# Kernel tuning notes

Measured on AMD Instinct MI355X. Metric: run time of the kernel, lower is better.

The kernel has to match this reference:

```python
import jax, jax.numpy as jnp
import numpy as np
import math

B, T, C, NH = 4, 2048, 1024, 16
HS = C // NH  # 64

def rope_cache(dim, max_pos):
    half = dim // 2
    inv_freq = 1.0 / (10000.0 ** (jnp.arange(half, dtype=jnp.float32) * 2.0 / dim))
    ang = jnp.arange(max_pos, dtype=jnp.float32)[:, None] * inv_freq[None, :]
    return jnp.cos(ang), jnp.sin(ang)  # each [T, half]

def apply_rope(x, cos, sin):
    # x: [B, nH, T, hs]; rotate consecutive pairs (complex multiply)
    x0 = x[..., 0::2]
    x1 = x[..., 1::2]
    c = cos[None, None, :, :]
    s = sin[None, None, :, :]
    r0 = x0 * c - x1 * s
    r1 = x0 * s + x1 * c
    return jnp.stack([r0, r1], axis=-1).reshape(x.shape)

def setup_inputs() -> dict:
    key = jax.random.key(0)
    ks = jax.random.split(key, 5)
    sc = 1.0 / math.sqrt(C)
    return {
        "x": jax.random.normal(ks[0], (B, T, C), jnp.float32),
        "Wq": jax.random.normal(ks[1], (C, C), jnp.float32) * sc,
        "bq": jnp.zeros((C,), jnp.float32),
        "Wk": jax.random.normal(ks[2], (C, C), jnp.float32) * sc,
        "bk": jnp.zeros((C,), jnp.float32),
        "Wv": jax.random.normal(ks[3], (C, C), jnp.float32) * sc,
        "bv": jnp.zeros((C,), jnp.float32),
        "Wp": jax.random.normal(ks[4], (C, C), jnp.float32) * sc,
        "bp": jnp.zeros((C,), jnp.float32),
    }

def reference(x, Wq, bq, Wk, bk, Wv, bv, Wp, bp):
    Bx, Tx, Cx = x.shape
    def split_heads(y):
        return y.reshape(Bx, Tx, NH, HS).transpose(0, 2, 1, 3)  # [B,nH,T,hs]
    q = split_heads(x @ Wq + bq)
    k = split_heads(x @ Wk + bk)
    v = split_heads(x @ Wv + bv)
    cos, sin = rope_cache(HS, Tx)
    q = apply_rope(q, cos, sin)
    k = apply_rope(k, cos, sin)
    att = jnp.einsum("bhqd,bhkd->bhqk", q, k) * (1.0 / math.sqrt(HS))
    causal = jnp.tril(jnp.ones((Tx, Tx), bool))
    att = jnp.where(causal[None, None, :, :], att, jnp.float32(-1e10))
    att = jax.nn.softmax(att, axis=-1)
    y = jnp.einsum("bhqk,bhkd->bhqd", att, v)
    y = y.transpose(0, 2, 1, 3).reshape(Bx, Tx, Cx)
    return y @ Wp + bp
```

## Files before the change

### kernel.cpp

```cpp
#include <hip/hip_runtime.h>
#include <math.h>

#define B_  4
#define T_  2048
#define C_  1024
#define NH_ 16
#define HS_ 64
#define M_  (B_ * T_)
#define BH_ (B_ * NH_)

typedef __bf16 bf16_t;
typedef __bf16 bf16x8 __attribute__((ext_vector_type(8)));
typedef float  f32x4  __attribute__((ext_vector_type(4)));

__device__ __forceinline__ f32x4 mfma16(bf16x8 a, bf16x8 b, f32x4 c) {
    return __builtin_amdgcn_mfma_f32_16x16x32_bf16(a, b, c, 0, 0, 0);
}

#define GLOAD16(gp, lp) __builtin_amdgcn_global_load_lds( \
    (const __attribute__((address_space(1))) void*)(gp),  \
    (__attribute__((address_space(3))) void*)(lp), 16, 0, 0)


__global__ void cvt_x(const float* __restrict__ x, bf16_t* __restrict__ xb) {
    int i = blockIdx.x * blockDim.x + threadIdx.x;
    const float4* src = reinterpret_cast<const float4*>(x);
    float4 u = src[2 * i], v = src[2 * i + 1];
    bf16x8 o;
    o[0] = (bf16_t)u.x; o[1] = (bf16_t)u.y; o[2] = (bf16_t)u.z; o[3] = (bf16_t)u.w;
    o[4] = (bf16_t)v.x; o[5] = (bf16_t)v.y; o[6] = (bf16_t)v.z; o[7] = (bf16_t)v.w;
    *reinterpret_cast<bf16x8*>(xb + (size_t)i * 8) = o;
}

__global__ void wtrans(const float* __restrict__ W, bf16_t* __restrict__ Wt) {
    __shared__ float tile[32][33];
    int bx = blockIdx.x, by = blockIdx.y;
    int tx = threadIdx.x, ty = threadIdx.y;
    #pragma unroll
    for (int j = 0; j < 4; ++j)
        tile[ty + j * 8][tx] = W[(size_t)(by * 32 + ty + j * 8) * 1024 + bx * 32 + tx];
    __syncthreads();
    #pragma unroll
    for (int j = 0; j < 4; ++j)
        Wt[(size_t)(bx * 32 + ty + j * 8) * 1024 + by * 32 + tx] = (bf16_t)tile[tx][ty + j * 8];
}

__global__ void rope_tab(float* __restrict__ cs, float* __restrict__ sn) {
    int idx = blockIdx.x * blockDim.x + threadIdx.x;
    int t = idx >> 5, j = idx & 31;
    float inv = 1.0f / powf(10000.0f, ((float)(2 * j)) / 64.0f);
    float ang = (float)t * inv;
    cs[idx] = cosf(ang);
    sn[idx] = sinf(ang);
}

__global__ __launch_bounds__(256) void gemm_qkv(
    const bf16_t* __restrict__ A, const bf16_t* __restrict__ Bt,
    const float* __restrict__ bq, const float* __restrict__ bk, const float* __restrict__ bv,
    bf16_t* __restrict__ outq, bf16_t* __restrict__ outk, bf16_t* __restrict__ outvt) {
    __shared__ __align__(16) bf16_t Ab[2][128 * 32];
    __shared__ __align__(16) bf16_t Bb[2][128 * 32];
    int tid = threadIdx.x;
    int lane = tid & 63, w = tid >> 6;
    int rr = lane & 15, g = lane >> 4;
    int mbase = blockIdx.y * 128;
    int nbase = blockIdx.x * 128;
    int wm = (w >> 1) * 64, wn = (w & 1) * 64;
    f32x4 acc[4][4] = {};
    int r0 = tid >> 2, c0 = tid & 3;
    const bf16_t* Asrc = A + (size_t)(mbase + r0) * 1024 + c0 * 8;
    const bf16_t* Bsrc = Bt + (size_t)(nbase + r0) * 1024 + c0 * 8;

    GLOAD16(Asrc,             &Ab[0][tid * 8]);
    GLOAD16(Asrc + 64 * 1024, &Ab[0][(tid + 256) * 8]);
    GLOAD16(Bsrc,             &Bb[0][tid * 8]);
    GLOAD16(Bsrc + 64 * 1024, &Bb[0][(tid + 256) * 8]);
    __syncthreads();
    int cur = 0;
    for (int t = 0; t < 32; ++t) {
        if (t < 31) {
            int kk = (t + 1) * 32;
            GLOAD16(Asrc + kk,             &Ab[cur ^ 1][tid * 8]);
            GLOAD16(Asrc + 64 * 1024 + kk, &Ab[cur ^ 1][(tid + 256) * 8]);
            GLOAD16(Bsrc + kk,             &Bb[cur ^ 1][tid * 8]);
            GLOAD16(Bsrc + 64 * 1024 + kk, &Bb[cur ^ 1][(tid + 256) * 8]);
        }
        bf16x8 a[4], b[4];
        #pragma unroll
        for (int i = 0; i < 4; ++i) {
            a[i] = *(const bf16x8*)&Ab[cur][(wm + i * 16 + rr) * 32 + g * 8];
            b[i] = *(const bf16x8*)&Bb[cur][(wn + i * 16 + rr) * 32 + g * 8];
        }
        #pragma unroll
        for (int mi = 0; mi < 4; ++mi)
            #pragma unroll
            for (int ni = 0; ni < 4; ++ni)
                acc[mi][ni] = mfma16(a[mi], b[ni], acc[mi][ni]);
        __syncthreads();
        cur ^= 1;
    }
    #pragma unroll
    for (int ni = 0; ni < 4; ++ni) {
        int n = nbase + wn + ni * 16 + rr;
        int sel = n >> 10, nn = n & 1023, h = nn >> 6, d = nn & 63;
        float bias = (sel == 0) ? bq[nn] : (sel == 1) ? bk[nn] : bv[nn];
        #pragma unroll
        for (int mi = 0; mi < 4; ++mi) {
            #pragma unroll
            for (int j = 0; j < 4; ++j) {
                int mrow = mbase + wm + mi * 16 + g * 4 + j;
                int bI = mrow >> 11, t = mrow & 2047;
                float val = acc[mi][ni][j] + bias;
                size_t bh = (size_t)(bI * 16 + h);
                if (sel == 0)      outq[(bh * 2048 + t) * 64 + d] = (bf16_t)val;
                else if (sel == 1) outk[(bh * 2048 + t) * 64 + d] = (bf16_t)val;
                else               outvt[(bh * 64 + d) * 2048 + t] = (bf16_t)val;
            }
        }
    }
}

__global__ void rope_qk(bf16_t* __restrict__ q, bf16_t* __restrict__ k,
                        const float* __restrict__ cs, const float* __restrict__ sn) {
    int idx = blockIdx.x * blockDim.x + threadIdx.x;
    int seg = idx & 7;
    int t = (idx >> 3) & 2047;
    int bh = idx >> 14;
    float4 cc = *reinterpret_cast<const float4*>(cs + (t << 5) + seg * 4);
    float4 ss = *reinterpret_cast<const float4*>(sn + (t << 5) + seg * 4);
    size_t base = (((size_t)bh << 11) + t) * 64 + seg * 8;
    {
        bf16x8 v = *reinterpret_cast<bf16x8*>(q + base);
        bf16x8 o;
        o[0] = (bf16_t)((float)v[0] * cc.x - (float)v[1] * ss.x);
        o[1] = (bf16_t)((float)v[0] * ss.x + (float)v[1] * cc.x);
        o[2] = (bf16_t)((float)v[2] * cc.y - (float)v[3] * ss.y);
        o[3] = (bf16_t)((float)v[2] * ss.y + (float)v[3] * cc.y);
        o[4] = (bf16_t)((float)v[4] * cc.z - (float)v[5] * ss.z);
        o[5] = (bf16_t)((float)v[4] * ss.z + (float)v[5] * cc.z);
        o[6] = (bf16_t)((float)v[6] * cc.w - (float)v[7] * ss.w);
        o[7] = (bf16_t)((float)v[6] * ss.w + (float)v[7] * cc.w);
        *reinterpret_cast<bf16x8*>(q + base) = o;
    }
    {
        bf16x8 v = *reinterpret_cast<bf16x8*>(k + base);
        bf16x8 o;
        o[0] = (bf16_t)((float)v[0] * cc.x - (float)v[1] * ss.x);
        o[1] = (bf16_t)((float)v[0] * ss.x + (float)v[1] * cc.x);
        o[2] = (bf16_t)((float)v[2] * cc.y - (float)v[3] * ss.y);
        o[3] = (bf16_t)((float)v[2] * ss.y + (float)v[3] * cc.y);
        o[4] = (bf16_t)((float)v[4] * cc.z - (float)v[5] * ss.z);
        o[5] = (bf16_t)((float)v[4] * ss.z + (float)v[5] * cc.z);
        o[6] = (bf16_t)((float)v[6] * cc.w - (float)v[7] * ss.w);
        o[7] = (bf16_t)((float)v[6] * ss.w + (float)v[7] * cc.w);
        *reinterpret_cast<bf16x8*>(k + base) = o;
    }
}

__global__ __launch_bounds__(256) void attn(
    const bf16_t* __restrict__ q, const bf16_t* __restrict__ k,
    const bf16_t* __restrict__ vt, bf16_t* __restrict__ y) {
    __shared__ __align__(16) bf16_t Kb[2][64 * 64];
    __shared__ __align__(16) bf16_t Vb[2][64 * 64];
    int tid = threadIdx.x;
    int lane = tid & 63, w = tid >> 6;
    int rr = lane & 15, g = lane >> 4;
    int bid = blockIdx.x;
    int xcd = bid & 7, idx = bid >> 3;
    int bh = xcd * 8 + (idx >> 4);
    int xp = idx & 15;
    const bf16_t* qh = q + (size_t)bh * T_ * HS_;
    const bf16_t* kh = k + (size_t)bh * T_ * HS_;
    const bf16_t* vh = vt + (size_t)bh * HS_ * T_;
    int bI = bh >> 4, h = bh & 15;
    int s0 = ((rr >> 2) << 3) + (rr & 3);
    const float SC = 0.125f * 1.44269504088896f;

    int i2a = tid, i2b = tid + 256;
    int rwa = i2a >> 3, rwb = i2b >> 3;
    int swKa = (rwa & 3) | (((rwa >> 3) & 1) << 2);
    int swKb = (rwb & 3) | (((rwb >> 3) & 1) << 2);
    int cKa = (i2a & 7) ^ swKa, cKb = (i2b & 7) ^ swKb;
    int cVa = (i2a & 7) ^ (rwa & 7), cVb = (i2b & 7) ^ (rwb & 7);

    #pragma unroll 1
    for (int pass = 0; pass < 2; ++pass) {
        int qt = pass ? (31 - xp) : xp;
        int qbase = qt * 64;
        int qrow = qbase + w * 16 + rr;
        bf16x8 qf0 = *reinterpret_cast<const bf16x8*>(qh + (size_t)qrow * 64 + g * 8);
        bf16x8 qf1 = *reinterpret_cast<const bf16x8*>(qh + (size_t)qrow * 64 + 32 + g * 8);
        float mrun = -1e30f, lsum = 0.f;
        f32x4 oacc[4] = {};
        int nt = qt + 1;
        GLOAD16(kh + (size_t)rwa * 64 + cKa * 8, &Kb[0][i2a * 8]);
        GLOAD16(kh + (size_t)rwb * 64 + cKb * 8, &Kb[0][i2b * 8]);
        GLOAD16(vh + (size_t)rwa * 2048 + cVa * 8, &Vb[0][i2a * 8]);
        GLOAD16(vh + (size_t)rwb * 2048 + cVb * 8, &Vb[0][i2b * 8]);
        __syncthreads();
        int cur = 0;
        #pragma unroll 1
        for (int t = 0; t < nt; ++t) {
            if (t + 1 < nt) {
                int kv1 = (t + 1) * 64;
                GLOAD16(kh + (size_t)(kv1 + rwa) * 64 + cKa * 8, &Kb[cur ^ 1][i2a * 8]);
                GLOAD16(kh + (size_t)(kv1 + rwb) * 64 + cKb * 8, &Kb[cur ^ 1][i2b * 8]);
                GLOAD16(vh + (size_t)rwa * 2048 + kv1 + cVa * 8, &Vb[cur ^ 1][i2a * 8]);
                GLOAD16(vh + (size_t)rwb * 2048 + kv1 + cVb * 8, &Vb[cur ^ 1][i2b * 8]);
            }
            int kv0 = t * 64;
            f32x4 st[4] = {};
            #pragma unroll
            for (int s = 0; s < 2; ++s) {
                #pragma unroll
                for (int p = 0; p < 2; ++p) {
                    int row = s * 32 + s0 + p * 4;
                    int sw = (row & 3) | (((row >> 3) & 1) << 2);
                    bf16x8 k0 = *(const bf16x8*)&Kb[cur][row * 64 + ((g ^ sw) * 8)];
                    bf16x8 k1 = *(const bf16x8*)&Kb[cur][row * 64 + (((4 + g) ^ sw) * 8)];
                    st[2 * s + p] = mfma16(k0, qf0, st[2 * s + p]);
                    st[2 * s + p] = mfma16(k1, qf1, st[2 * s + p]);
                }
            }
            float sv[16];
            #pragma unroll
            for (int s = 0; s < 2; ++s)
                #pragma unroll
                for (int p = 0; p < 2; ++p)
                    #pragma unroll
                    for (int j = 0; j < 4; ++j)
                        sv[s * 8 + p * 4 + j] = st[2 * s + p][j] * SC;
            if (t == nt - 1) {
                #pragma unroll
                for (int i = 0; i < 16; ++i) {
                    int kvi = kv0 + (i >> 3) * 32 + g * 8 + (i & 7);
                    if (kvi > qrow) sv[i] = -1e30f;
                }
            }
            float pmax = sv[0];
            #pragma unroll
            for (int i = 1; i < 16; ++i) pmax = fmaxf(pmax, sv[i]);
            pmax = fmaxf(pmax, __shfl_xor(pmax, 16));
            pmax = fmaxf(pmax, __shfl_xor(pmax, 32));
            float mnew = fmaxf(mrun, pmax);
            float fac = __builtin_amdgcn_exp2f(mrun - mnew);
            float psum = 0.f;
            bf16x8 pf0, pf1;
            #pragma unroll
            for (int i = 0; i < 8; ++i) {
                float pe = __builtin_amdgcn_exp2f(sv[i] - mnew);
                psum += pe;
                pf0[i] = (bf16_t)pe;
            }
            #pragma unroll
            for (int i = 0; i < 8; ++i) {
                float pe = __builtin_amdgcn_exp2f(sv[8 + i] - mnew);
                psum += pe;
                pf1[i] = (bf16_t)pe;
            }
            psum += __shfl_xor(psum, 16);
            psum += __shfl_xor(psum, 32);
            lsum = lsum * fac + psum;
            mrun = mnew;
            #pragma unroll
            for (int ch = 0; ch < 4; ++ch) {
                #pragma unroll
                for (int j = 0; j < 4; ++j) oacc[ch][j] *= fac;
            }
            #pragma unroll
            for (int ch = 0; ch < 4; ++ch) {
                int row = ch * 16 + rr;
                bf16x8 v0 = *(const bf16x8*)&Vb[cur][row * 64 + ((g ^ (row & 7)) * 8)];
                bf16x8 v1 = *(const bf16x8*)&Vb[cur][row * 64 + (((4 + g) ^ (row & 7)) * 8)];
                oacc[ch] = mfma16(v0, pf0, oacc[ch]);
                oacc[ch] = mfma16(v1, pf1, oacc[ch]);
            }
            __syncthreads();
            cur ^= 1;
        }
        float inv = 1.0f / lsum;
        bf16_t* yrow = y + ((size_t)bI * 2048 + qrow) * 1024 + h * 64;
        #pragma unroll
        for (int ch = 0; ch < 4; ++ch) {
            union { bf16_t b[4]; short4 s4; } u;
            #pragma unroll
            for (int j = 0; j < 4; ++j) u.b[j] = (bf16_t)(oacc[ch][j] * inv);
            *reinterpret_cast<short4*>(yrow + ch * 16 + g * 4) = u.s4;
        }
    }
}

__global__ __launch_bounds__(256) void gemm_proj(
    const bf16_t* __restrict__ A, const bf16_t* __restrict__ Bt,
    const float* __restrict__ bp, float* __restrict__ out) {
    __shared__ __align__(16) bf16_t Ab[2][128 * 32];
    __shared__ __align__(16) bf16_t Bb[2][128 * 32];
    int tid = threadIdx.x;
    int lane = tid & 63, w = tid >> 6;
    int rr = lane & 15, g = lane >> 4;
    int mbase = blockIdx.y * 128;
    int nbase = blockIdx.x * 128;
    int wm = (w >> 1) * 64, wn = (w & 1) * 64;
    f32x4 acc[4][4] = {};
    int r0 = tid >> 2, c0 = tid & 3;
    const bf16_t* Asrc = A + (size_t)(mbase + r0) * 1024 + c0 * 8;
    const bf16_t* Bsrc = Bt + (size_t)(nbase + r0) * 1024 + c0 * 8;

    GLOAD16(Asrc,             &Ab[0][tid * 8]);
    GLOAD16(Asrc + 64 * 1024, &Ab[0][(tid + 256) * 8]);
    GLOAD16(Bsrc,             &Bb[0][tid * 8]);
    GLOAD16(Bsrc + 64 * 1024, &Bb[0][(tid + 256) * 8]);
    __syncthreads();
    int cur = 0;
    for (int t = 0; t < 32; ++t) {
        if (t < 31) {
            int kk = (t + 1) * 32;
            GLOAD16(Asrc + kk,             &Ab[cur ^ 1][tid * 8]);
            GLOAD16(Asrc + 64 * 1024 + kk, &Ab[cur ^ 1][(tid + 256) * 8]);
            GLOAD16(Bsrc + kk,             &Bb[cur ^ 1][tid * 8]);
            GLOAD16(Bsrc + 64 * 1024 + kk, &Bb[cur ^ 1][(tid + 256) * 8]);
        }
        bf16x8 a[4], b[4];
        #pragma unroll
        for (int i = 0; i < 4; ++i) {
            a[i] = *(const bf16x8*)&Ab[cur][(wm + i * 16 + rr) * 32 + g * 8];
            b[i] = *(const bf16x8*)&Bb[cur][(wn + i * 16 + rr) * 32 + g * 8];
        }
        #pragma unroll
        for (int mi = 0; mi < 4; ++mi)
            #pragma unroll
            for (int ni = 0; ni < 4; ++ni)
                acc[mi][ni] = mfma16(a[mi], b[ni], acc[mi][ni]);
        __syncthreads();
        cur ^= 1;
    }
    #pragma unroll
    for (int ni = 0; ni < 4; ++ni) {
        int n = nbase + wn + ni * 16 + rr;
        float bias = bp[n];
        #pragma unroll
        for (int mi = 0; mi < 4; ++mi) {
            #pragma unroll
            for (int j = 0; j < 4; ++j) {
                int mrow = mbase + wm + mi * 16 + g * 4 + j;
                out[(size_t)mrow * 1024 + n] = acc[mi][ni][j] + bias;
            }
        }
    }
}

extern "C" void kernel_launch(void* const* d_in, const int* in_sizes, int n_in,
                              void* d_out, int out_size, void* d_ws, size_t ws_size,
                              hipStream_t stream) {
    const float* x  = (const float*)d_in[0];
    const float* Wq = (const float*)d_in[1];
    const float* bq = (const float*)d_in[2];
    const float* Wk = (const float*)d_in[3];
    const float* bk = (const float*)d_in[4];
    const float* Wv = (const float*)d_in[5];
    const float* bv = (const float*)d_in[6];
    const float* Wp = (const float*)d_in[7];
    const float* bp = (const float*)d_in[8];
    float* out = (float*)d_out;

    char* p = (char*)d_ws;
    auto alloc = [&](size_t n) { char* r = p; p += (n + 255) & ~(size_t)255; return r; };
    bf16_t* xb    = (bf16_t*)alloc((size_t)M_ * C_ * 2);
    bf16_t* wtqkv = (bf16_t*)alloc((size_t)3 * C_ * C_ * 2);
    bf16_t* wtp   = (bf16_t*)alloc((size_t)C_ * C_ * 2);
    bf16_t* qb    = (bf16_t*)alloc((size_t)BH_ * T_ * HS_ * 2);
    bf16_t* kb    = (bf16_t*)alloc((size_t)BH_ * T_ * HS_ * 2);
    bf16_t* vtb   = (bf16_t*)alloc((size_t)BH_ * HS_ * T_ * 2);
    bf16_t* yb    = (bf16_t*)alloc((size_t)M_ * C_ * 2);
    float*  cs    = (float*)alloc((size_t)T_ * 32 * 4);
    float*  sn    = (float*)alloc((size_t)T_ * 32 * 4);

    cvt_x<<<4096, 256, 0, stream>>>(x, xb);
    wtrans<<<dim3(32, 32), dim3(32, 8), 0, stream>>>(Wq, wtqkv);
    wtrans<<<dim3(32, 32), dim3(32, 8), 0, stream>>>(Wk, wtqkv + (size_t)C_ * C_);
    wtrans<<<dim3(32, 32), dim3(32, 8), 0, stream>>>(Wv, wtqkv + (size_t)2 * C_ * C_);
    wtrans<<<dim3(32, 32), dim3(32, 8), 0, stream>>>(Wp, wtp);
    rope_tab<<<256, 256, 0, stream>>>(cs, sn);

    gemm_qkv<<<dim3(24, 64), 256, 0, stream>>>(xb, wtqkv, bq, bk, bv, qb, kb, vtb);
    rope_qk<<<4096, 256, 0, stream>>>(qb, kb, cs, sn);
    attn<<<1024, 256, 0, stream>>>(qb, kb, vtb, yb);
    gemm_proj<<<dim3(8, 64), 256, 0, stream>>>(yb, wtp, bp, out);
}
```

Baseline: 326.1 us.

## Enlarge GEMM tiles to 256x128x64 with XOR-swizzled LDS and block remapping

Both the QKV and projection GEMMs move to 512-thread blocks computing 256x128 output tiles with a K-step of 64 instead of 32. The LDS layout is XOR-swizzled by row to avoid bank conflicts, and the linear block index is remapped so that neighbouring blocks share operand tiles in L2. The aim is more operand reuse per byte loaded, half as many barriers, and fewer LDS conflicts. In exchange the kernels use much more shared memory (96KB per block), which may limit occupancy, and the wm/wn mapping with 8 warps needs checking for correctness.

```diff
diff --git a/kernel.cpp b/kernel.cpp
--- a/kernel.cpp
+++ b/kernel.cpp
@@ -54,48 +54,57 @@
     sn[idx] = sinf(ang);
 }
 
-__global__ __launch_bounds__(256) void gemm_qkv(
+__global__ __launch_bounds__(512) void gemm_qkv(
     const bf16_t* __restrict__ A, const bf16_t* __restrict__ Bt,
     const float* __restrict__ bq, const float* __restrict__ bk, const float* __restrict__ bv,
     bf16_t* __restrict__ outq, bf16_t* __restrict__ outk, bf16_t* __restrict__ outvt) {
-    __shared__ __align__(16) bf16_t Ab[2][128 * 32];
-    __shared__ __align__(16) bf16_t Bb[2][128 * 32];
+    __shared__ __align__(16) bf16_t Ab[2][256 * 64];
+    __shared__ __align__(16) bf16_t Bb[2][128 * 64];
     int tid = threadIdx.x;
     int lane = tid & 63, w = tid >> 6;
     int rr = lane & 15, g = lane >> 4;
-    int mbase = blockIdx.y * 128;
-    int nbase = blockIdx.x * 128;
+    int lin = blockIdx.y * 24 + blockIdx.x;
+    int swz = (lin & 7) * 96 + (lin >> 3);
+    int bx = swz % 24, by = swz / 24;
+    int mbase = by * 256, nbase = bx * 128;
     int wm = (w >> 1) * 64, wn = (w & 1) * 64;
+    int rA = tid >> 3;
+    int cS = (tid & 7) ^ (rA & 7);
+    const bf16_t* Asrc = A + (size_t)(mbase + rA) * 1024 + cS * 8;
+    const bf16_t* Bsrc = Bt + (size_t)(nbase + rA) * 1024 + cS * 8;
+    int r7 = rr & 7;
+    int ch0 = ((0 + g) ^ r7) * 8, ch1 = ((4 + g) ^ r7) * 8;
     f32x4 acc[4][4] = {};
-    int r0 = tid >> 2, c0 = tid & 3;
-    const bf16_t* Asrc = A + (size_t)(mbase + r0) * 1024 + c0 * 8;
-    const bf16_t* Bsrc = Bt + (size_t)(nbase + r0) * 1024 + c0 * 8;
-
-    GLOAD16(Asrc,             &Ab[0][tid * 8]);
-    GLOAD16(Asrc + 64 * 1024, &Ab[0][(tid + 256) * 8]);
-    GLOAD16(Bsrc,             &Bb[0][tid * 8]);
-    GLOAD16(Bsrc + 64 * 1024, &Bb[0][(tid + 256) * 8]);
+
+    #pragma unroll
+    for (int j = 0; j < 4; ++j) GLOAD16(Asrc + (size_t)j * 64 * 1024, &Ab[0][tid * 8 + j * 4096]);
+    #pragma unroll
+    for (int j = 0; j < 2; ++j) GLOAD16(Bsrc + (size_t)j * 64 * 1024, &Bb[0][tid * 8 + j * 4096]);
     __syncthreads();
     int cur = 0;
-    for (int t = 0; t < 32; ++t) {
-        if (t < 31) {
-            int kk = (t + 1) * 32;
-            GLOAD16(Asrc + kk,             &Ab[cur ^ 1][tid * 8]);
-            GLOAD16(Asrc + 64 * 1024 + kk, &Ab[cur ^ 1][(tid + 256) * 8]);
-            GLOAD16(Bsrc + kk,             &Bb[cur ^ 1][tid * 8]);
-            GLOAD16(Bsrc + 64 * 1024 + kk, &Bb[cur ^ 1][(tid + 256) * 8]);
-        }
-        bf16x8 a[4], b[4];
+    for (int t = 0; t < 16; ++t) {
+        if (t < 15) {
+            int kk = (t + 1) * 64;
+            #pragma unroll
+            for (int j = 0; j < 4; ++j) GLOAD16(Asrc + kk + (size_t)j * 64 * 1024, &Ab[cur ^ 1][tid * 8 + j * 4096]);
+            #pragma unroll
+            for (int j = 0; j < 2; ++j) GLOAD16(Bsrc + kk + (size_t)j * 64 * 1024, &Bb[cur ^ 1][tid * 8 + j * 4096]);
+        }
         #pragma unroll
-        for (int i = 0; i < 4; ++i) {
-            a[i] = *(const bf16x8*)&Ab[cur][(wm + i * 16 + rr) * 32 + g * 8];
-            b[i] = *(const bf16x8*)&Bb[cur][(wn + i * 16 + rr) * 32 + g * 8];
-        }
-        #pragma unroll
-        for (int mi = 0; mi < 4; ++mi)
-            #pragma unroll
-            for (int ni = 0; ni < 4; ++ni)
-                acc[mi][ni] = mfma16(a[mi], b[ni], acc[mi][ni]);
+        for (int kk = 0; kk < 2; ++kk) {
+            int co = kk ? ch1 : ch0;
+            bf16x8 a[4], b[4];
+            #pragma unroll
+            for (int i = 0; i < 4; ++i) {
+                a[i] = *(const bf16x8*)&Ab[cur][(wm + i * 16 + rr) * 64 + co];
+                b[i] = *(const bf16x8*)&Bb[cur][(wn + i * 16 + rr) * 64 + co];
+            }
+            #pragma unroll
+            for (int mi = 0; mi < 4; ++mi)
+                #pragma unroll
+                for (int ni = 0; ni < 4; ++ni)
+                    acc[mi][ni] = mfma16(a[mi], b[ni], acc[mi][ni]);
+        }
         __syncthreads();
         cur ^= 1;
     }
@@ -290,47 +299,56 @@
     }
 }
 
-__global__ __launch_bounds__(256) void gemm_proj(
+__global__ __launch_bounds__(512) void gemm_proj(
     const bf16_t* __restrict__ A, const bf16_t* __restrict__ Bt,
     const float* __restrict__ bp, float* __restrict__ out) {
-    __shared__ __align__(16) bf16_t Ab[2][128 * 32];
-    __shared__ __align__(16) bf16_t Bb[2][128 * 32];
+    __shared__ __align__(16) bf16_t Ab[2][256 * 64];
+    __shared__ __align__(16) bf16_t Bb[2][128 * 64];
     int tid = threadIdx.x;
     int lane = tid & 63, w = tid >> 6;
     int rr = lane & 15, g = lane >> 4;
-    int mbase = blockIdx.y * 128;
-    int nbase = blockIdx.x * 128;
+    int lin = blockIdx.y * 8 + blockIdx.x;
+    int swz = (lin & 7) * 32 + (lin >> 3);
+    int bx = swz % 8, by = swz / 8;
+    int mbase = by * 256, nbase = bx * 128;
     int wm = (w >> 1) * 64, wn = (w & 1) * 64;
+    int rA = tid >> 3;
+    int cS = (tid & 7) ^ (rA & 7);
+    const bf16_t* Asrc = A + (size_t)(mbase + rA) * 1024 + cS * 8;
+    const bf16_t* Bsrc = Bt + (size_t)(nbase + rA) * 1024 + cS * 8;
+    int r7 = rr & 7;
+    int ch0 = ((0 + g) ^ r7) * 8, ch1 = ((4 + g) ^ r7) * 8;
     f32x4 acc[4][4] = {};
-    int r0 = tid >> 2, c0 = tid & 3;
-    const bf16_t* Asrc = A + (size_t)(mbase + r0) * 1024 + c0 * 8;
-    const bf16_t* Bsrc = Bt + (size_t)(nbase + r0) * 1024 + c0 * 8;
-
-    GLOAD16(Asrc,             &Ab[0][tid * 8]);
-    GLOAD16(Asrc + 64 * 1024, &Ab[0][(tid + 256) * 8]);
-    GLOAD16(Bsrc,             &Bb[0][tid * 8]);
-    GLOAD16(Bsrc + 64 * 1024, &Bb[0][(tid + 256) * 8]);
+
+    #pragma unroll
+    for (int j = 0; j < 4; ++j) GLOAD16(Asrc + (size_t)j * 64 * 1024, &Ab[0][tid * 8 + j * 4096]);
+    #pragma unroll
+    for (int j = 0; j < 2; ++j) GLOAD16(Bsrc + (size_t)j * 64 * 1024, &Bb[0][tid * 8 + j * 4096]);
     __syncthreads();
     int cur = 0;
-    for (int t = 0; t < 32; ++t) {
-        if (t < 31) {
-            int kk = (t + 1) * 32;
-            GLOAD16(Asrc + kk,             &Ab[cur ^ 1][tid * 8]);
-            GLOAD16(Asrc + 64 * 1024 + kk, &Ab[cur ^ 1][(tid + 256) * 8]);
-            GLOAD16(Bsrc + kk,             &Bb[cur ^ 1][tid * 8]);
-            GLOAD16(Bsrc + 64 * 1024 + kk, &Bb[cur ^ 1][(tid + 256) * 8]);
-        }
-        bf16x8 a[4], b[4];
+    for (int t = 0; t < 16; ++t) {
+        if (t < 15) {
+            int kk = (t + 1) * 64;
+            #pragma unroll
+            for (int j = 0; j < 4; ++j) GLOAD16(Asrc + kk + (size_t)j * 64 * 1024, &Ab[cur ^ 1][tid * 8 + j * 4096]);
+            #pragma unroll
+            for (int j = 0; j < 2; ++j) GLOAD16(Bsrc + kk + (size_t)j * 64 * 1024, &Bb[cur ^ 1][tid * 8 + j * 4096]);
+        }
         #pragma unroll
-        for (int i = 0; i < 4; ++i) {
-            a[i] = *(const bf16x8*)&Ab[cur][(wm + i * 16 + rr) * 32 + g * 8];
-            b[i] = *(const bf16x8*)&Bb[cur][(wn + i * 16 + rr) * 32 + g * 8];
-        }
-        #pragma unroll
-        for (int mi = 0; mi < 4; ++mi)
-            #pragma unroll
-            for (int ni = 0; ni < 4; ++ni)
-                acc[mi][ni] = mfma16(a[mi], b[ni], acc[mi][ni]);
+        for (int kk = 0; kk < 2; ++kk) {
+            int co = kk ? ch1 : ch0;
+            bf16x8 a[4], b[4];
+            #pragma unroll
+            for (int i = 0; i < 4; ++i) {
+                a[i] = *(const bf16x8*)&Ab[cur][(wm + i * 16 + rr) * 64 + co];
+                b[i] = *(const bf16x8*)&Bb[cur][(wn + i * 16 + rr) * 64 + co];
+            }
+            #pragma unroll
+            for (int mi = 0; mi < 4; ++mi)
+                #pragma unroll
+                for (int ni = 0; ni < 4; ++ni)
+                    acc[mi][ni] = mfma16(a[mi], b[ni], acc[mi][ni]);
+        }
         __syncthreads();
         cur ^= 1;
     }
@@ -382,8 +400,8 @@
     wtrans<<<dim3(32, 32), dim3(32, 8), 0, stream>>>(Wp, wtp);
     rope_tab<<<256, 256, 0, stream>>>(cs, sn);
 
-    gemm_qkv<<<dim3(24, 64), 256, 0, stream>>>(xb, wtqkv, bq, bk, bv, qb, kb, vtb);
+    gemm_qkv<<<dim3(24, 32), 512, 0, stream>>>(xb, wtqkv, bq, bk, bv, qb, kb, vtb);
     rope_qk<<<4096, 256, 0, stream>>>(qb, kb, cs, sn);
     attn<<<1024, 256, 0, stream>>>(qb, kb, vtb, yb);
-    gemm_proj<<<dim3(8, 64), 256, 0, stream>>>(yb, wtp, bp, out);
-}
+    gemm_proj<<<dim3(8, 32), 512, 0, stream>>>(yb, wtp, bp, out);
+}
```

Result: faster. 318.7 us (-2.3%).
